# Kernel tuning notes

Hardware: AMD Instinct MI355X
Metric: run time of the kernel (lower is better)

The kernel has to match this reference:

```python
import jax, jax.numpy as jnp
import numpy as np

B, S = 4096, 128
POS_RANK, DIR_RANK = 10, 4
WIDTH = 256
POS_DIM = POS_RANK * 6  # 60
DIR_DIM = DIR_RANK * 6  # 24
SKIPS = (4,)


def _pe(x, rank):
    # x: [N, 3] -> [N, 6*rank]; sin/cos of x scaled by 2^i for i in 0..rank-1
    freqs = (2.0 ** jnp.arange(rank)).astype(x.dtype)        # [L]
    xf = x[..., None] * freqs                                 # [N, 3, L]
    enc = jnp.concatenate([jnp.sin(xf), jnp.cos(xf)], axis=-1)  # [N, 3, 2L]
    return enc.reshape(x.shape[0], -1)


def _linear_init(key, fan_in, fan_out):
    k1, k2 = jax.random.split(key)
    bound = 1.0 / np.sqrt(fan_in)
    W = jax.random.uniform(k1, (fan_in, fan_out), jnp.float32, -bound, bound)
    b = jax.random.uniform(k2, (fan_out,), jnp.float32, -bound, bound)
    return W, b


def setup_inputs() -> dict:
    key = jax.random.key(0)
    ks = jax.random.split(key, 16)
    inp = {
        "input_pos": jax.random.normal(ks[0], (B, S, 3), jnp.float32),
        "input_dir": jax.random.normal(ks[1], (B, S, 3), jnp.float32),
    }
    # trunk layers: in-dims follow skip-concat structure
    in_dims = [POS_DIM] + [WIDTH + POS_DIM if (i in SKIPS) else WIDTH for i in range(7)]
    for i, d_in in enumerate(in_dims):
        W, b = _linear_init(ks[2 + i], d_in, WIDTH)
        inp[f"W{i}"] = W
        inp[f"b{i}"] = b
    inp["Wd"], inp["bd"] = _linear_init(ks[10], WIDTH, 1)
    inp["Wc0"], inp["bc0"] = _linear_init(ks[11], WIDTH + DIR_DIM, WIDTH // 2)
    inp["Wc1"], inp["bc1"] = _linear_init(ks[12], WIDTH // 2, 3)
    return inp


def reference(input_pos, input_dir,
              W0, b0, W1, b1, W2, b2, W3, b3, W4, b4, W5, b5, W6, b6, W7, b7,
              Wd, bd, Wc0, bc0, Wc1, bc1):
    Ws = [W0, W1, W2, W3, W4, W5, W6, W7]
    bs = [b0, b1, b2, b3, b4, b5, b6, b7]
    b, s, _ = input_pos.shape
    embed_pos = _pe(input_pos.reshape(-1, 3), POS_RANK)  # [N, 60]
    embed_dir = _pe(input_dir.reshape(-1, 3), DIR_RANK)  # [N, 24]
    hx = embed_pos
    for i, (W, bb) in enumerate(zip(Ws, bs)):
        hx = jax.nn.relu(hx @ W + bb)
        if i in SKIPS:
            hx = jnp.concatenate([hx, embed_pos], axis=1)
    density = (hx @ Wd + bd).reshape(b, s)
    dir_feat = jnp.concatenate([hx, embed_dir], axis=1)  # [N, 280]
    color = (jax.nn.relu(dir_feat @ Wc0 + bc0) @ Wc1 + bc1).reshape(b, s, 3)
    return density, color
```

## Files before the change

kernel.cpp:

```cpp
#include <hip/hip_runtime.h>
#include <hip/hip_bf16.h>

using bf16 = __bf16;
typedef __bf16 bf16x8 __attribute__((ext_vector_type(8)));
typedef __bf16 bf16x4 __attribute__((ext_vector_type(4)));
typedef float  f32x4  __attribute__((ext_vector_type(4)));

#define MFMA16(a, b, c) __builtin_amdgcn_mfma_f32_16x16x32_bf16((a), (b), (c), 0, 0, 0)

constexpr int P0  = 0;
constexpr int P1  = 16384;
constexpr int P2  = 81920;
constexpr int P3  = 147456;
constexpr int P4  = 212992;
constexpr int P5  = 278528;
constexpr int P6  = 360448;
constexpr int P7  = 425984;
constexpr int PD  = 491520;
constexpr int PC0 = 495616;
constexpr int PC1 = 532480;

constexpr int NPTS = 4096 * 128;
constexpr int SH = 328;

struct PackArgs {
    const float* src[11];
    int K[11], N[11], Ntiles[11], tasks[11], dstoff[11];
};

__global__ void nerf_pack(PackArgs pa, bf16* __restrict__ dst) {
    int idx = blockIdx.x * 256 + threadIdx.x;
    for (int l = 0; l < 11; ++l) {
        if (idx < pa.tasks[l]) {
            const int lane = idx & 63;
            const int blk  = idx >> 6;
            const int nt   = blk % pa.Ntiles[l];
            const int kt   = blk / pa.Ntiles[l];
            const int kb   = kt * 32 + (lane >> 4) * 8;
            const int n    = nt * 16 + (lane & 15);
            const float* s = pa.src[l];
            const int K = pa.K[l], N = pa.N[l];
            bf16x8 v;
#pragma unroll
            for (int j = 0; j < 8; ++j) {
                int k = kb + j;
                v[j] = (bf16)((k < K && n < N) ? s[(size_t)k * N + n] : 0.f);
            }
            *(bf16x8*)(dst + pa.dstoff[l] + (size_t)idx * 8) = v;
            return;
        }
        idx -= pa.tasks[l];
    }
}

template <int KP, int N, bool RELU, int MODE, bool HAZARD>
__device__ __forceinline__ void layer(const bf16* src, bf16* H,
                                      const bf16* __restrict__ wp,
                                      const float* __restrict__ bias,
                                      float* __restrict__ gout, int m0) {
    constexpr int NTILES = N / 16;
    constexpr int NT_W   = (NTILES < 4) ? NTILES : 4;
    constexpr int CG     = NTILES / NT_W;
    constexpr int PT_W   = CG;

    const int tid  = threadIdx.x;
    const int lane = tid & 63;
    const int w    = tid >> 6;
    const int l15  = lane & 15;
    const int quad = lane >> 4;
    const int nt0  = (w % CG) * NT_W;
    const int pt0  = (w / CG) * PT_W;

    f32x4 bias4[NT_W];
    if constexpr (MODE == 0) {
#pragma unroll
        for (int nt = 0; nt < NT_W; ++nt)
            bias4[nt] = *(const f32x4*)(bias + (nt0 + nt) * 16 + quad * 4);
    } else if constexpr (MODE == 1) {
        const float bv = bias[0];
        f32x4 t = {bv, bv, bv, bv}; bias4[0] = t;
    } else {
        f32x4 t = {bias[0], bias[1], bias[2], 0.f}; bias4[0] = t;
    }

    f32x4 acc[PT_W][NT_W];
#pragma unroll
    for (int pt = 0; pt < PT_W; ++pt)
#pragma unroll
        for (int nt = 0; nt < NT_W; ++nt) acc[pt][nt] = bias4[nt];

#pragma unroll 2
    for (int kt = 0; kt < KP / 32; ++kt) {
        bf16x8 wf[NT_W];
#pragma unroll
        for (int nt = 0; nt < NT_W; ++nt)
            wf[nt] = *(const bf16x8*)(wp + ((size_t)(kt * NTILES + nt0 + nt) * 64 + lane) * 8);
#pragma unroll
        for (int pt = 0; pt < PT_W; ++pt) {
            const int point = (pt0 + pt) * 16 + l15;
            bf16x8 af = *(const bf16x8*)(src + point * SH + kt * 32 + quad * 8);
#pragma unroll
            for (int nt = 0; nt < NT_W; ++nt)
                acc[pt][nt] = MFMA16(wf[nt], af, acc[pt][nt]);
        }
    }
    if (HAZARD) __syncthreads();

    if constexpr (MODE == 0) {
#pragma unroll
        for (int pt = 0; pt < PT_W; ++pt) {
            const int point = (pt0 + pt) * 16 + l15;
#pragma unroll
            for (int nt = 0; nt < NT_W; ++nt) {
                f32x4 a = acc[pt][nt];
                bf16x4 o;
#pragma unroll
                for (int r = 0; r < 4; ++r) {
                    float v = a[r];
                    if (RELU) v = v > 0.f ? v : 0.f;
                    o[r] = (bf16)v;
                }
                *(bf16x4*)(H + point * SH + (nt0 + nt) * 16 + quad * 4) = o;
            }
        }
        __syncthreads();
    } else if constexpr (MODE == 1) {
        if (quad == 0) gout[m0 + pt0 * 16 + l15] = acc[0][0][0];
    } else {
        if (quad == 0) {
            const size_t p3 = (size_t)(m0 + pt0 * 16 + l15) * 3;
            gout[p3 + 0] = acc[0][0][0];
            gout[p3 + 1] = acc[0][0][1];
            gout[p3 + 2] = acc[0][0][2];
        }
    }
}

__global__ __launch_bounds__(256, 3)
void nerf_main(const float* __restrict__ pos, const float* __restrict__ dir,
               const float* __restrict__ b0, const float* __restrict__ b1,
               const float* __restrict__ b2, const float* __restrict__ b3,
               const float* __restrict__ b4, const float* __restrict__ b5,
               const float* __restrict__ b6, const float* __restrict__ b7,
               const float* __restrict__ bd, const float* __restrict__ bc0,
               const float* __restrict__ bc1,
               const bf16* __restrict__ wpk, float* __restrict__ out) {
    __shared__ __align__(16) bf16 H[64 * SH];

    const int m0 = blockIdx.x * 64;

    H[(threadIdx.x & 63) * SH + 316 + (threadIdx.x >> 6)] = (bf16)0.f;

    {
        const int row = threadIdx.x >> 2;
        const int cg  = threadIdx.x & 3;
        const size_t pb = (size_t)(m0 + row) * 3;
        float xs[3] = { pos[pb], pos[pb + 1], pos[pb + 2] };
#pragma unroll
        for (int j = 0; j < 15; ++j) {
            const int col = cg * 15 + j;
            const int c = col / 20, rem = col % 20, s = rem / 10, i = rem % 10;
            const float arg = xs[c] * (float)(1 << i);
            float v = s ? __cosf(arg) : __sinf(arg);
            H[row * SH + 256 + col] = (bf16)v;
        }
    }
    __syncthreads();

    layer<64,  256, true, 0, false>(H + 256, H, wpk + P0, b0, nullptr, m0);
    layer<256, 256, true, 0, true >(H, H, wpk + P1, b1, nullptr, m0);
    layer<256, 256, true, 0, true >(H, H, wpk + P2, b2, nullptr, m0);
    layer<256, 256, true, 0, true >(H, H, wpk + P3, b3, nullptr, m0);
    layer<256, 256, true, 0, true >(H, H, wpk + P4, b4, nullptr, m0);
    layer<320, 256, true, 0, true >(H, H, wpk + P5, b5, nullptr, m0);
    layer<256, 256, true, 0, true >(H, H, wpk + P6, b6, nullptr, m0);
    layer<256, 256, true, 0, true >(H, H, wpk + P7, b7, nullptr, m0);

    layer<256, 16, false, 1, false>(H, H, wpk + PD, bd, out, m0);

    {
        const int row = threadIdx.x >> 2;
        const int cg  = threadIdx.x & 3;
        const size_t db = (size_t)(m0 + row) * 3;
        float ds[3] = { dir[db], dir[db + 1], dir[db + 2] };
#pragma unroll
        for (int j = 0; j < 8; ++j) {
            const int col = cg * 8 + j;
            float v = 0.f;
            if (col < 24) {
                const int c = col / 8, rem = col % 8, s = rem / 4, i = rem % 4;
                const float arg = ds[c] * (float)(1 << i);
                v = s ? __cosf(arg) : __sinf(arg);
            }
            H[row * SH + 256 + col] = (bf16)v;
        }
    }
    __syncthreads();

    layer<288, 128, true, 0, true >(H, H, wpk + PC0, bc0, nullptr, m0);
    layer<128, 16, false, 2, false>(H, H, wpk + PC1, bc1, out + NPTS, m0);
}

__global__ void nerf_sentinel(float* __restrict__ out, float val) {
    if (threadIdx.x == 0 && blockIdx.x == 0) out[0] = val;
}

extern "C" void kernel_launch(void* const* d_in, const int* in_sizes, int n_in,
                              void* d_out, int out_size, void* d_ws, size_t ws_size,
                              hipStream_t stream) {
    static const int exp2[24] = {
        1572864, 1572864,
        15360, 256, 65536, 256, 65536, 256, 65536, 256,
        65536, 256, 80896, 256, 65536, 256, 65536, 256,
        256, 1, 35840, 128, 384, 3
    };
    int bad = -1;
    if (n_in != 24) bad = 99;
    else {
        for (int i = 0; i < 24; ++i)
            if (in_sizes[i] != exp2[i]) { bad = i; break; }
    }
    if (bad < 0 && out_size != NPTS * 4) bad = 97;
    if (bad >= 0) {
        nerf_sentinel<<<1, 64, 0, stream>>>((float*)d_out, 20000.f + 100.f * bad);
        return;
    }

    static const int wi[11] = {2, 4, 6, 8, 10, 12, 14, 16, 18, 20, 22};
    static const int Ks[11] = {60, 256, 256, 256, 256, 316, 256, 256, 256, 280, 128};
    static const int Ns[11] = {256, 256, 256, 256, 256, 256, 256, 256, 1, 128, 3};
    static const int Kp[11] = {64, 256, 256, 256, 256, 320, 256, 256, 256, 288, 128};
    static const int Np[11] = {256, 256, 256, 256, 256, 256, 256, 256, 16, 128, 16};

    PackArgs pa;
    int off = 0, total_tasks = 0;
    for (int l = 0; l < 11; ++l) {
        pa.src[l]    = (const float*)d_in[wi[l]];
        pa.K[l]      = Ks[l];
        pa.N[l]      = Ns[l];
        pa.Ntiles[l] = Np[l] / 16;
        pa.tasks[l]  = (Kp[l] / 32) * (Np[l] / 16) * 64;
        pa.dstoff[l] = off;
        off += pa.tasks[l] * 8;
        total_tasks += pa.tasks[l];
    }
    bf16* wpk = (bf16*)d_ws;

    nerf_pack<<<(total_tasks + 255) / 256, 256, 0, stream>>>(pa, wpk);

    nerf_main<<<NPTS / 64, 256, 0, stream>>>(
        (const float*)d_in[0], (const float*)d_in[1],
        (const float*)d_in[3], (const float*)d_in[5], (const float*)d_in[7],
        (const float*)d_in[9], (const float*)d_in[11], (const float*)d_in[13],
        (const float*)d_in[15], (const float*)d_in[17], (const float*)d_in[19],
        (const float*)d_in[21], (const float*)d_in[23],
        wpk, (float*)d_out);
}
```

Before: 604.4 us.

## Use 2-wave blocks with larger per-wave MFMA tiles for more register reuse

```diff
diff --git a/kernel.cpp b/kernel.cpp
--- a/kernel.cpp
+++ b/kernel.cpp
@@ -59,9 +59,10 @@
                                       const float* __restrict__ bias,
                                       float* __restrict__ gout, int m0) {
     constexpr int NTILES = N / 16;
-    constexpr int NT_W   = (NTILES < 4) ? NTILES : 4;
+    constexpr int NT_W   = (NTILES < 8) ? NTILES : 8;
     constexpr int CG     = NTILES / NT_W;
-    constexpr int PT_W   = CG;
+    constexpr int NPG    = 2 / CG;
+    constexpr int PT_W   = 4 / NPG;
 
     const int tid  = threadIdx.x;
     const int lane = tid & 63;
@@ -71,23 +72,24 @@
     const int nt0  = (w % CG) * NT_W;
     const int pt0  = (w / CG) * PT_W;
 
-    f32x4 bias4[NT_W];
+    f32x4 acc[PT_W][NT_W];
     if constexpr (MODE == 0) {
 #pragma unroll
-        for (int nt = 0; nt < NT_W; ++nt)
-            bias4[nt] = *(const f32x4*)(bias + (nt0 + nt) * 16 + quad * 4);
+        for (int nt = 0; nt < NT_W; ++nt) {
+            f32x4 b4 = *(const f32x4*)(bias + (nt0 + nt) * 16 + quad * 4);
+#pragma unroll
+            for (int pt = 0; pt < PT_W; ++pt) acc[pt][nt] = b4;
+        }
     } else if constexpr (MODE == 1) {
         const float bv = bias[0];
-        f32x4 t = {bv, bv, bv, bv}; bias4[0] = t;
+        f32x4 t = {bv, bv, bv, bv};
+#pragma unroll
+        for (int pt = 0; pt < PT_W; ++pt) acc[pt][0] = t;
     } else {
-        f32x4 t = {bias[0], bias[1], bias[2], 0.f}; bias4[0] = t;
-    }
-
-    f32x4 acc[PT_W][NT_W];
-#pragma unroll
-    for (int pt = 0; pt < PT_W; ++pt)
-#pragma unroll
-        for (int nt = 0; nt < NT_W; ++nt) acc[pt][nt] = bias4[nt];
+        f32x4 t = {bias[0], bias[1], bias[2], 0.f};
+#pragma unroll
+        for (int pt = 0; pt < PT_W; ++pt) acc[pt][0] = t;
+    }
 
 #pragma unroll 2
     for (int kt = 0; kt < KP / 32; ++kt) {
@@ -125,18 +127,25 @@
         }
         __syncthreads();
     } else if constexpr (MODE == 1) {
-        if (quad == 0) gout[m0 + pt0 * 16 + l15] = acc[0][0][0];
+        if (quad == 0) {
+#pragma unroll
+            for (int pt = 0; pt < PT_W; ++pt)
+                gout[m0 + (pt0 + pt) * 16 + l15] = acc[pt][0][0];
+        }
     } else {
         if (quad == 0) {
-            const size_t p3 = (size_t)(m0 + pt0 * 16 + l15) * 3;
-            gout[p3 + 0] = acc[0][0][0];
-            gout[p3 + 1] = acc[0][0][1];
-            gout[p3 + 2] = acc[0][0][2];
-        }
-    }
-}
-
-__global__ __launch_bounds__(256, 3)
+#pragma unroll
+            for (int pt = 0; pt < PT_W; ++pt) {
+                const size_t p3 = (size_t)(m0 + (pt0 + pt) * 16 + l15) * 3;
+                gout[p3 + 0] = acc[pt][0][0];
+                gout[p3 + 1] = acc[pt][0][1];
+                gout[p3 + 2] = acc[pt][0][2];
+            }
+        }
+    }
+}
+
+__global__ __launch_bounds__(128, 2)
 void nerf_main(const float* __restrict__ pos, const float* __restrict__ dir,
                const float* __restrict__ b0, const float* __restrict__ b1,
                const float* __restrict__ b2, const float* __restrict__ b3,
@@ -148,17 +157,18 @@
     __shared__ __align__(16) bf16 H[64 * SH];
 
     const int m0 = blockIdx.x * 64;
-
-    H[(threadIdx.x & 63) * SH + 316 + (threadIdx.x >> 6)] = (bf16)0.f;
+    const int tid = threadIdx.x;
+
+    *(unsigned int*)(H + (tid & 63) * SH + 316 + 2 * (tid >> 6)) = 0u;
 
     {
-        const int row = threadIdx.x >> 2;
-        const int cg  = threadIdx.x & 3;
+        const int row  = tid >> 1;
+        const int half = tid & 1;
         const size_t pb = (size_t)(m0 + row) * 3;
         float xs[3] = { pos[pb], pos[pb + 1], pos[pb + 2] };
 #pragma unroll
-        for (int j = 0; j < 15; ++j) {
-            const int col = cg * 15 + j;
+        for (int j = 0; j < 30; ++j) {
+            const int col = half * 30 + j;
             const int c = col / 20, rem = col % 20, s = rem / 10, i = rem % 10;
             const float arg = xs[c] * (float)(1 << i);
             float v = s ? __cosf(arg) : __sinf(arg);
@@ -179,21 +189,19 @@
     layer<256, 16, false, 1, false>(H, H, wpk + PD, bd, out, m0);
 
     {
-        const int row = threadIdx.x >> 2;
-        const int cg  = threadIdx.x & 3;
+        const int row  = tid >> 1;
+        const int half = tid & 1;
         const size_t db = (size_t)(m0 + row) * 3;
         float ds[3] = { dir[db], dir[db + 1], dir[db + 2] };
 #pragma unroll
-        for (int j = 0; j < 8; ++j) {
-            const int col = cg * 8 + j;
-            float v = 0.f;
-            if (col < 24) {
-                const int c = col / 8, rem = col % 8, s = rem / 4, i = rem % 4;
-                const float arg = ds[c] * (float)(1 << i);
-                v = s ? __cosf(arg) : __sinf(arg);
-            }
+        for (int j = 0; j < 12; ++j) {
+            const int col = half * 12 + j;
+            const int c = col / 8, rem = col % 8, s = rem / 4, i = rem % 4;
+            const float arg = ds[c] * (float)(1 << i);
+            float v = s ? __cosf(arg) : __sinf(arg);
             H[row * SH + 256 + col] = (bf16)v;
         }
+        *(unsigned long long*)(H + row * SH + 280 + half * 4) = 0ull;
     }
     __syncthreads();
 
@@ -248,7 +256,7 @@
 
     nerf_pack<<<(total_tasks + 255) / 256, 256, 0, stream>>>(pa, wpk);
 
-    nerf_main<<<NPTS / 64, 256, 0, stream>>>(
+    nerf_main<<<NPTS / 64, 128, 0, stream>>>(
         (const float*)d_in[0], (const float*)d_in[1],
         (const float*)d_in[3], (const float*)d_in[5], (const float*)d_in[7],
         (const float*)d_in[9], (const float*)d_in[11], (const float*)d_in[13],
```

New measurement: 645.3 us. 6.8% more time.
